# Kernel tuning notes

Measured on AMD Instinct MI355X. Metric: run time of the kernel, lower is better.

The kernel has to match this reference:

```python
import jax, jax.numpy as jnp
import numpy as np

B, S, D, H, DH = 2, 2048, 768, 12, 64
GAMMA = 0.5
SMOOTHING = 1.0  # softmax_attn_smoothing scalar (non-trainable weight in the original)
SCALE = 1.0 / float(np.sqrt(DH))


def setup_inputs() -> dict:
    key = jax.random.key(0)
    ks = jax.random.split(key, 8)
    w = 0.02
    return {
        "inp": jax.random.normal(ks[0], (B, S, D), dtype=jnp.float32),
        "pos_emb": jax.random.normal(ks[1], (S, D), dtype=jnp.float32),
        "Wq_inp": jax.random.normal(ks[2], (D, H * DH), dtype=jnp.float32) * w,
        "Wk_inp": jax.random.normal(ks[3], (D, H * DH), dtype=jnp.float32) * w,
        "Wq_pos": jax.random.normal(ks[4], (D, H * DH), dtype=jnp.float32) * w,
        "Wk_pos": jax.random.normal(ks[5], (D, H * DH), dtype=jnp.float32) * w,
        "Wv": jax.random.normal(ks[6], (D, H * DH), dtype=jnp.float32) * w,
        "Wo": jax.random.normal(ks[7], (H * DH, D), dtype=jnp.float32) * w,
    }


def reference(inp, pos_emb, Wq_inp, Wk_inp, Wq_pos, Wk_pos, Wv, Wo):
    # projections; note original reshape order: [..., d_head, n_head]
    q_i = (inp @ Wq_inp).reshape(B, S, DH, H)
    k_i = (inp @ Wk_inp).reshape(B, S, DH, H)
    q_p = (pos_emb @ Wq_pos).reshape(S, DH, H)
    k_p = (pos_emb @ Wk_pos).reshape(S, DH, H)
    v = (inp @ Wv).reshape(B, S, DH, H)

    # content-content stream: [B,S,S,H], softmax over key axis (axis=2)
    score_inp = jnp.einsum("bidh,bjdh->bijh", q_i, k_i) * (SCALE * SMOOTHING)
    prob_inp = jax.nn.softmax(score_inp, axis=2)

    # position-position stream: [S,S,H], softmax over key axis (axis=1)
    score_pos = jnp.einsum("idh,jdh->ijh", q_p, k_p) * (SCALE * SMOOTHING)
    prob_pos = jax.nn.softmax(score_pos, axis=1)[None]  # [1,S,S,H]

    # gamma blend of the two attention distributions
    attn_prob = (1.0 - GAMMA) * prob_inp + GAMMA * prob_pos  # [B,S,S,H]

    # V-weighted sum, merge heads as [..., h, d] per the original 'bihd' output
    attn_out = jnp.einsum("bijh,bjdh->bihd", attn_prob, v).reshape(B, S, H * DH)
    attn_out = attn_out @ Wo  # [B,S,D]
    return attn_out, attn_prob
```

## Files before the change

### kernel.cpp

```cpp
#include <hip/hip_runtime.h>
#include <hip/hip_bf16.h>

constexpr int NH  = 12;
constexpr int SEQ = 2048;
constexpr int DHD = 64;
constexpr int DIM = 768;
constexpr float QSCALE = 0.125f * 1.44269504088896f;

typedef __bf16 bf16x8 __attribute__((ext_vector_type(8)));
typedef __bf16 bf16x4 __attribute__((ext_vector_type(4)));
typedef float  f32x4  __attribute__((ext_vector_type(4)));

#define MFMA16(a, b, c) __builtin_amdgcn_mfma_f32_16x16x32_bf16((a), (b), (c), 0, 0, 0)

#define LGKM_BARRIER() asm volatile("s_waitcnt lgkmcnt(0)\n\ts_barrier" ::: "memory")

__global__ __launch_bounds__(256) void conv_kernel(
    const float* __restrict__ inp, const float* __restrict__ pos,
    __bf16* __restrict__ Ab, __bf16* __restrict__ Pb)
{
    const int idx = blockIdx.x * 256 + threadIdx.x;
    constexpr int N8I = 4096 * 768 / 8;
    constexpr int N8P = 2048 * 768 / 8;
    if (idx >= N8I + N8P) return;
    const float* src; __bf16* dst; int off;
    if (idx < N8I) { src = inp; dst = Ab; off = idx; }
    else           { src = pos; dst = Pb; off = idx - N8I; }
    const float4 v0 = *reinterpret_cast<const float4*>(&src[(size_t)off * 8]);
    const float4 v1 = *reinterpret_cast<const float4*>(&src[(size_t)off * 8 + 4]);
    bf16x8 t;
    t[0] = (__bf16)v0.x; t[1] = (__bf16)v0.y; t[2] = (__bf16)v0.z; t[3] = (__bf16)v0.w;
    t[4] = (__bf16)v1.x; t[5] = (__bf16)v1.y; t[6] = (__bf16)v1.z; t[7] = (__bf16)v1.w;
    *reinterpret_cast<bf16x8*>(&dst[(size_t)off * 8]) = t;
}

__global__ __launch_bounds__(256) void packw_kernel(
    const float* __restrict__ Wqi, const float* __restrict__ Wki,
    const float* __restrict__ Wvv, const float* __restrict__ Wqp,
    const float* __restrict__ Wkp, __bf16* __restrict__ Wp)
{
    const int kt = blockIdx.x, h = blockIdx.y, z = blockIdx.z;
    const int k0 = kt * 64;
    const float* W; float scale = 1.0f;
    if (z == 0)      { W = Wqi; scale = QSCALE; }
    else if (z == 1) { W = Wki; }
    else if (z == 2) { W = Wvv; }
    else if (z == 3) { W = Wqp; scale = QSCALE; }
    else             { W = Wkp; }

    __shared__ __bf16 lds[64][68];
    const int tid = threadIdx.x;
    {
        const int d = tid & 63, kq = tid >> 6;
        #pragma unroll
        for (int rep = 0; rep < 16; ++rep) {
            const int kk = rep * 4 + kq;
            lds[kk][d] = (__bf16)(W[(size_t)(k0 + kk) * DIM + d * 12 + h] * scale);
        }
    }
    __syncthreads();
    {
        const int k = tid & 63, dq = tid >> 6;
        const size_t slab = ((size_t)z * 12 + h) * 64;
        #pragma unroll
        for (int rep = 0; rep < 16; ++rep) {
            const int d = rep * 4 + dq;
            Wp[(slab + d) * DIM + k0 + k] = lds[k][d];
        }
    }
}

__global__ __launch_bounds__(256) void proj_kernel(
    const __bf16* __restrict__ Ab, const __bf16* __restrict__ Pb,
    const __bf16* __restrict__ Wp,
    __bf16* __restrict__ Qi, __bf16* __restrict__ Ki, __bf16* __restrict__ Vsd,
    __bf16* __restrict__ Qp, __bf16* __restrict__ Kp)
{
    const int bx = blockIdx.x, h = blockIdx.y, z = blockIdx.z;
    if (z >= 3 && bx >= 8) return;
    const int tid = threadIdx.x, lane = tid & 63, wv = tid >> 6;
    const int l15 = lane & 15, lg = lane >> 4;
    const int m_w = bx * 256 + wv * 64;

    const __bf16* Asrc = (z < 3) ? Ab : Pb;
    const __bf16* Wsl = Wp + ((size_t)z * 12 + h) * 64 * DIM;

    f32x4 acc[4][4] = {};

    for (int kt = 0; kt < 24; ++kt) {
        const int k0 = kt * 32;
        bf16x8 a[4], b[4];
        #pragma unroll
        for (int mf = 0; mf < 4; ++mf)
            a[mf] = *reinterpret_cast<const bf16x8*>(
                &Asrc[(size_t)(m_w + mf * 16 + l15) * DIM + k0 + lg * 8]);
        #pragma unroll
        for (int nf = 0; nf < 4; ++nf)
            b[nf] = *reinterpret_cast<const bf16x8*>(
                &Wsl[(size_t)(nf * 16 + l15) * DIM + k0 + lg * 8]);
        #pragma unroll
        for (int mf = 0; mf < 4; ++mf)
            #pragma unroll
            for (int nf = 0; nf < 4; ++nf)
                acc[mf][nf] = MFMA16(a[mf], b[nf], acc[mf][nf]);
    }

    __bf16* outp = (z == 0) ? Qi : (z == 1) ? Ki : (z == 2) ? Vsd : (z == 3) ? Qp : Kp;
    #pragma unroll
    for (int mf = 0; mf < 4; ++mf)
        #pragma unroll
        for (int r = 0; r < 4; ++r) {
            const int m = m_w + mf * 16 + lg * 4 + r;
            const int s = m & 2047;
            const int slab = (z < 3) ? ((m >> 11) * 12 + h) : h;
            const size_t base = ((size_t)slab * SEQ + s) * DHD;
            #pragma unroll
            for (int nf = 0; nf < 4; ++nf)
                outp[base + nf * 16 + l15] = (__bf16)acc[mf][nf][r];
        }
}

__global__ __launch_bounds__(256) void vtrans_kernel(
    const __bf16* __restrict__ Vsd, __bf16* __restrict__ Vt)
{
    const int s0 = blockIdx.x * 64, slab = blockIdx.y;
    __shared__ __bf16 lds[64][66];
    const int tid = threadIdx.x;
    {
        const int rr = tid >> 3, cq = tid & 7;
        #pragma unroll
        for (int rep = 0; rep < 2; ++rep) {
            const int r2 = rr + rep * 32;
            *reinterpret_cast<bf16x8*>(&lds[r2][cq * 8]) =
                *reinterpret_cast<const bf16x8*>(
                    &Vsd[((size_t)slab * SEQ + s0 + r2) * DHD + cq * 8]);
        }
    }
    __syncthreads();
    {
        const int dd = tid >> 3, sq = tid & 7;
        #pragma unroll
        for (int rep = 0; rep < 2; ++rep) {
            const int d2 = dd + rep * 32;
            bf16x8 v;
            #pragma unroll
            for (int q = 0; q < 8; ++q) v[q] = lds[sq * 8 + q][d2];
            *reinterpret_cast<bf16x8*>(&Vt[((size_t)slab * DHD + d2) * SEQ + s0 + sq * 8]) = v;
        }
    }
}

__global__ __launch_bounds__(64) void stats_kernel(
    const __bf16* __restrict__ Qi, const __bf16* __restrict__ Ki,
    const __bf16* __restrict__ Qp, const __bf16* __restrict__ Kp,
    float* __restrict__ m_ws, float* __restrict__ l_ws)
{
    const int bid = blockIdx.x + 128 * (blockIdx.y + 12 * blockIdx.z);
    const int wg = (bid & 7) * 576 + (bid >> 3);
    const int bx = wg & 127, h = (wg >> 7) % 12, bb = wg / 1536;

    const int lane = threadIdx.x;
    const int l15 = lane & 15, lg = lane >> 4;
    const int i0 = bx * 16;

    const __bf16* Q = (bb < 2) ? Qi + ((size_t)bb * NH + h) * SEQ * DHD
                               : Qp + (size_t)h * SEQ * DHD;
    const __bf16* K = (bb < 2) ? Ki + ((size_t)bb * NH + h) * SEQ * DHD
                               : Kp + (size_t)h * SEQ * DHD;

    bf16x8 a[2];
    #pragma unroll
    for (int ks = 0; ks < 2; ++ks)
        a[ks] = *reinterpret_cast<const bf16x8*>(
            &Q[(size_t)(i0 + l15) * DHD + ks * 32 + lg * 8]);

    float mr[4], lr[4];
    #pragma unroll
    for (int r = 0; r < 4; ++r) { mr[r] = -1e30f; lr[r] = 0.0f; }

    for (int jt = 0; jt < 32; ++jt) {
        const int j0 = jt * 64;
        bf16x8 bk[2][4];
        #pragma unroll
        for (int ks = 0; ks < 2; ++ks)
            #pragma unroll
            for (int nf = 0; nf < 4; ++nf)
                bk[ks][nf] = *reinterpret_cast<const bf16x8*>(
                    &K[(size_t)(j0 + nf * 16 + l15) * DHD + ks * 32 + lg * 8]);
        f32x4 c[4] = {};
        #pragma unroll
        for (int ks = 0; ks < 2; ++ks)
            #pragma unroll
            for (int nf = 0; nf < 4; ++nf)
                c[nf] = MFMA16(a[ks], bk[ks][nf], c[nf]);

        #pragma unroll
        for (int r = 0; r < 4; ++r) {
            const float x01 = fmaxf(c[0][r], c[1][r]);
            const float x23 = fmaxf(c[2][r], c[3][r]);
            const float mn = fmaxf(mr[r], fmaxf(x01, x23));
            lr[r] = lr[r] * exp2f(mr[r] - mn)
                  + exp2f(c[0][r] - mn) + exp2f(c[1][r] - mn)
                  + exp2f(c[2][r] - mn) + exp2f(c[3][r] - mn);
            mr[r] = mn;
        }
    }

    #pragma unroll
    for (int msk = 1; msk < 16; msk <<= 1)
        #pragma unroll
        for (int r = 0; r < 4; ++r) {
            const float mo = __shfl_xor(mr[r], msk);
            const float lo = __shfl_xor(lr[r], msk);
            const float mn = fmaxf(mr[r], mo);
            lr[r] = lr[r] * exp2f(mr[r] - mn) + lo * exp2f(mo - mn);
            mr[r] = mn;
        }

    if (l15 == 0) {
        const size_t base = ((size_t)bb * NH + h) * SEQ + i0;
        #pragma unroll
        for (int r = 0; r < 4; ++r) {
            m_ws[base + lg * 4 + r] = mr[r];
            l_ws[base + lg * 4 + r] = lr[r];
        }
    }
}

__global__ __launch_bounds__(384) void emit_kernel(
    const __bf16* __restrict__ Qi, const __bf16* __restrict__ Ki,
    const __bf16* __restrict__ Qp, const __bf16* __restrict__ Kp,
    const __bf16* __restrict__ Vt,
    const float* __restrict__ m_ws, const float* __restrict__ l_ws,
    float* __restrict__ out1, float* __restrict__ attn_pre)
{
    const int bid = blockIdx.x + 128 * (blockIdx.y + 4 * blockIdx.z);
    const int wg = (bid & 7) * 128 + (bid >> 3);
    const int it = wg & 127, js = (wg >> 7) & 3, b = wg >> 9;

    const int i0 = it * 16;
    const int tid = threadIdx.x, lane = tid & 63, wv = tid >> 6;
    const int l15 = lane & 15, lg = lane >> 4;

    __shared__ __align__(16) __bf16 ppv[12][16][40];
    __shared__ __align__(16) __bf16 pb2[16][32][12];
    __shared__ float ml[12][16][4];
    const __bf16* p2flat = &pb2[0][0][0];

    if (tid < 192) {
        const int h = tid >> 4, i = tid & 15;
        const size_t bi  = ((size_t)b * NH + h) * SEQ + i0 + i;
        const size_t ppi = ((size_t)2 * NH + h) * SEQ + i0 + i;
        ml[h][i][0] = m_ws[bi];
        ml[h][i][1] = 0.5f / l_ws[bi];
        ml[h][i][2] = m_ws[ppi];
        ml[h][i][3] = 0.5f / l_ws[ppi];
    }
    __syncthreads();

    const __bf16* Kb[2][2];
    bf16x8 aQ[2][2][2];
    #pragma unroll
    for (int hh = 0; hh < 2; ++hh) {
        const int h = wv * 2 + hh;
        Kb[hh][0] = Ki + ((size_t)b * NH + h) * SEQ * DHD;
        Kb[hh][1] = Kp + (size_t)h * SEQ * DHD;
        #pragma unroll
        for (int ks = 0; ks < 2; ++ks) {
            aQ[hh][0][ks] = *reinterpret_cast<const bf16x8*>(
                &Qi[(((size_t)b * NH + h) * SEQ + i0 + l15) * DHD + ks * 32 + lg * 8]);
            aQ[hh][1][ks] = *reinterpret_cast<const bf16x8*>(
                &Qp[((size_t)h * SEQ + i0 + l15) * DHD + ks * 32 + lg * 8]);
        }
    }

    bf16x8 kf[2][2][2][2];
    {
        const int j0 = js * 512;
        #pragma unroll
        for (int hh = 0; hh < 2; ++hh)
            #pragma unroll
            for (int st = 0; st < 2; ++st)
                #pragma unroll
                for (int nf = 0; nf < 2; ++nf)
                    #pragma unroll
                    for (int ks = 0; ks < 2; ++ks)
                        kf[hh][st][nf][ks] = *reinterpret_cast<const bf16x8*>(
                            &Kb[hh][st][(size_t)(j0 + nf * 16 + l15) * DHD + ks * 32 + lg * 8]);
    }

    f32x4 acc[2][4] = {};

    #pragma unroll 1
    for (int jt = 0; jt < 16; ++jt) {
        const int j0 = js * 512 + jt * 32;
        const int jn = (js * 512 + (jt + 1) * 32) & (SEQ - 1);

        f32x4 ci[2][2] = {}, cq[2][2] = {};
        #pragma unroll
        for (int hh = 0; hh < 2; ++hh)
            #pragma unroll
            for (int ks = 0; ks < 2; ++ks)
                #pragma unroll
                for (int nf = 0; nf < 2; ++nf) {
                    ci[hh][nf] = MFMA16(aQ[hh][0][ks], kf[hh][0][nf][ks], ci[hh][nf]);
                    cq[hh][nf] = MFMA16(aQ[hh][1][ks], kf[hh][1][nf][ks], cq[hh][nf]);
                }

        #pragma unroll
        for (int hh = 0; hh < 2; ++hh)
            #pragma unroll
            for (int st = 0; st < 2; ++st)
                #pragma unroll
                for (int nf = 0; nf < 2; ++nf)
                    #pragma unroll
                    for (int ks = 0; ks < 2; ++ks)
                        kf[hh][st][nf][ks] = *reinterpret_cast<const bf16x8*>(
                            &Kb[hh][st][(size_t)(jn + nf * 16 + l15) * DHD + ks * 32 + lg * 8]);

        #pragma unroll
        for (int hh = 0; hh < 2; ++hh) {
            const int h = wv * 2 + hh;
            #pragma unroll
            for (int r = 0; r < 4; ++r) {
                const int i = lg * 4 + r;
                const f32x4 mlv = *reinterpret_cast<const f32x4*>(&ml[h][i][0]);
                #pragma unroll
                for (int nf = 0; nf < 2; ++nf) {
                    const float pi_ = exp2f(ci[hh][nf][r] - mlv[0]) * mlv[1];
                    const float pq_ = exp2f(cq[hh][nf][r] - mlv[2]) * mlv[3];
                    const __bf16 p = (__bf16)(pi_ + pq_);
                    const int jj = nf * 16 + l15;
                    ppv[h][i][jj] = p;
                    pb2[i][jj][h] = p;
                }
            }
        }

        #pragma unroll
        for (int hh = 0; hh < 2; ++hh) {
            const int h = wv * 2 + hh;
            const bf16x8 ap = *reinterpret_cast<const bf16x8*>(&ppv[h][l15][lg * 8]);
            #pragma unroll
            for (int nf = 0; nf < 4; ++nf) {
                const bf16x8 bv = *reinterpret_cast<const bf16x8*>(
                    &Vt[(((size_t)b * NH + h) * DHD + nf * 16 + l15) * SEQ + j0 + lg * 8]);
                acc[hh][nf] = MFMA16(ap, bv, acc[hh][nf]);
            }
        }

        LGKM_BARRIER();

        #pragma unroll
        for (int k = 0; k < 4; ++k) {
            const int o = (wv * 4 + k) * 256 + 4 * lane;
            const int i = o / 384;
            const int rem = o - i * 384;
            const bf16x4 pv4 = *reinterpret_cast<const bf16x4*>(&p2flat[o]);
            f32x4 v;
            #pragma unroll
            for (int q = 0; q < 4; ++q) v[q] = (float)pv4[q];
            const size_t addr = ((size_t)(b * SEQ + i0 + i) * SEQ + j0) * 12 + rem;
            *reinterpret_cast<f32x4*>(&out1[addr]) = v;
        }

        LGKM_BARRIER();
    }

    #pragma unroll
    for (int hh = 0; hh < 2; ++hh) {
        const int h = wv * 2 + hh;
        #pragma unroll
        for (int nf = 0; nf < 4; ++nf)
            #pragma unroll
            for (int r = 0; r < 4; ++r) {
                const int i = lg * 4 + r;
                atomicAdd(&attn_pre[((size_t)(b * SEQ + i0 + i)) * DIM + h * DHD + nf * 16 + l15],
                          acc[hh][nf][r]);
            }
    }
}

__global__ __launch_bounds__(256) void final_kernel(
    const float* __restrict__ A, const float* __restrict__ W, float* __restrict__ out0)
{
    const int m0 = blockIdx.y * 64;
    const int n0 = blockIdx.x * 192;

    __shared__ __bf16 Al[64][32];
    __shared__ __bf16 Wl[192][32];

    const int tid = threadIdx.x;
    const int lane = tid & 63, wv = tid >> 6;
    const int wm = wv >> 1, wn = wv & 1;
    const int l15 = lane & 15, lg = lane >> 4;

    f32x4 c[2][6] = {};

    for (int kt = 0; kt < 24; ++kt) {
        const int k0 = kt * 32;
        __syncthreads();
        {
            const int r = tid >> 3, kq = tid & 7;
            #pragma unroll
            for (int rep = 0; rep < 2; ++rep) {
                const float4 v = *reinterpret_cast<const float4*>(
                    &A[(size_t)(m0 + r + rep * 32) * DIM + k0 + kq * 4]);
                bf16x4 t;
                t[0] = (__bf16)v.x; t[1] = (__bf16)v.y; t[2] = (__bf16)v.z; t[3] = (__bf16)v.w;
                *reinterpret_cast<bf16x4*>(&Al[r + rep * 32][kq * 4]) = t;
            }
        }
        for (int idx = tid; idx < 32 * 48; idx += 256) {
            const int k = idx / 48, nq = idx - k * 48;
            const float4 v = *reinterpret_cast<const float4*>(
                &W[(size_t)(k0 + k) * DIM + n0 + nq * 4]);
            Wl[nq * 4 + 0][k] = (__bf16)v.x;
            Wl[nq * 4 + 1][k] = (__bf16)v.y;
            Wl[nq * 4 + 2][k] = (__bf16)v.z;
            Wl[nq * 4 + 3][k] = (__bf16)v.w;
        }
        __syncthreads();

        bf16x8 a[2], b[6];
        #pragma unroll
        for (int mf = 0; mf < 2; ++mf)
            a[mf] = *reinterpret_cast<const bf16x8*>(&Al[wm * 32 + mf * 16 + l15][lg * 8]);
        #pragma unroll
        for (int nf = 0; nf < 6; ++nf)
            b[nf] = *reinterpret_cast<const bf16x8*>(&Wl[wn * 96 + nf * 16 + l15][lg * 8]);
        #pragma unroll
        for (int mf = 0; mf < 2; ++mf)
            #pragma unroll
            for (int nf = 0; nf < 6; ++nf)
                c[mf][nf] = MFMA16(a[mf], b[nf], c[mf][nf]);
    }

    #pragma unroll
    for (int mf = 0; mf < 2; ++mf)
        #pragma unroll
        for (int nf = 0; nf < 6; ++nf)
            #pragma unroll
            for (int r = 0; r < 4; ++r) {
                const int m = m0 + wm * 32 + mf * 16 + lg * 4 + r;
                const int n = n0 + wn * 96 + nf * 16 + l15;
                out0[(size_t)m * DIM + n] = c[mf][nf][r];
            }
}

extern "C" void kernel_launch(void* const* d_in, const int* in_sizes, int n_in,
                              void* d_out, int out_size, void* d_ws, size_t ws_size,
                              hipStream_t stream)
{
    (void)in_sizes; (void)n_in; (void)out_size; (void)ws_size;

    const float* inp = (const float*)d_in[0];
    const float* pos = (const float*)d_in[1];
    const float* Wqi = (const float*)d_in[2];
    const float* Wki = (const float*)d_in[3];
    const float* Wqp = (const float*)d_in[4];
    const float* Wkp = (const float*)d_in[5];
    const float* Wvv = (const float*)d_in[6];
    const float* Wo  = (const float*)d_in[7];

    char* w = (char*)d_ws;
    __bf16* Ab = (__bf16*)w;  w += (size_t)4096 * 768 * 2;
    __bf16* Pb = (__bf16*)w;  w += (size_t)2048 * 768 * 2;
    __bf16* Wp = (__bf16*)w;  w += (size_t)5 * 768 * 768 * 2;
    __bf16* Qi = (__bf16*)w;  w += (size_t)2 * NH * SEQ * DHD * 2;
    __bf16* Ki = (__bf16*)w;  w += (size_t)2 * NH * SEQ * DHD * 2;
    __bf16* Vsd = (__bf16*)w; w += (size_t)2 * NH * SEQ * DHD * 2;
    __bf16* Qp = (__bf16*)w;  w += (size_t)NH * SEQ * DHD * 2;
    __bf16* Kp = (__bf16*)w;  w += (size_t)NH * SEQ * DHD * 2;
    float* m_ws = (float*)w;  w += (size_t)3 * NH * SEQ * 4;
    float* l_ws = (float*)w;  w += (size_t)3 * NH * SEQ * 4;
    float* attn_pre = (float*)w; w += (size_t)4096 * DIM * 4;
    __bf16* Vt = Ab;

    float* out0 = (float*)d_out;
    float* out1 = out0 + (size_t)2 * SEQ * DIM;

    hipMemsetAsync(attn_pre, 0, (size_t)4096 * DIM * 4, stream);

    hipLaunchKernelGGL(conv_kernel, dim3(2304), dim3(256), 0, stream, inp, pos, Ab, Pb);
    hipLaunchKernelGGL(packw_kernel, dim3(12, 12, 5), dim3(256), 0, stream,
                       Wqi, Wki, Wvv, Wqp, Wkp, Wp);
    hipLaunchKernelGGL(proj_kernel, dim3(16, 12, 5), dim3(256), 0, stream,
                       Ab, Pb, Wp, Qi, Ki, Vsd, Qp, Kp);
    hipLaunchKernelGGL(vtrans_kernel, dim3(32, 24), dim3(256), 0, stream, Vsd, Vt);
    hipLaunchKernelGGL(stats_kernel, dim3(128, 12, 3), dim3(64), 0, stream,
                       Qi, Ki, Qp, Kp, m_ws, l_ws);
    hipLaunchKernelGGL(emit_kernel, dim3(128, 4, 2), dim3(384), 0, stream,
                       Qi, Ki, Qp, Kp, Vt, m_ws, l_ws, out1, attn_pre);
    hipLaunchKernelGGL(final_kernel, dim3(4, 64, 1), dim3(256), 0, stream,
                       attn_pre, Wo, out0);
}
```

Measured before the change: 718.3 us.

## Split probability emission and PV accumulation into separate kernels

```diff
diff --git a/kernel.cpp b/kernel.cpp
--- a/kernel.cpp
+++ b/kernel.cpp
@@ -12,8 +12,6 @@
 typedef float  f32x4  __attribute__((ext_vector_type(4)));
 
 #define MFMA16(a, b, c) __builtin_amdgcn_mfma_f32_16x16x32_bf16((a), (b), (c), 0, 0, 0)
-
-#define LGKM_BARRIER() asm volatile("s_waitcnt lgkmcnt(0)\n\ts_barrier" ::: "memory")
 
 __global__ __launch_bounds__(256) void conv_kernel(
     const float* __restrict__ inp, const float* __restrict__ pos,
@@ -227,25 +225,23 @@
     }
 }
 
-__global__ __launch_bounds__(384) void emit_kernel(
+__global__ __launch_bounds__(256) void emit_kernel(
     const __bf16* __restrict__ Qi, const __bf16* __restrict__ Ki,
     const __bf16* __restrict__ Qp, const __bf16* __restrict__ Kp,
-    const __bf16* __restrict__ Vt,
     const float* __restrict__ m_ws, const float* __restrict__ l_ws,
-    float* __restrict__ out1, float* __restrict__ attn_pre)
-{
-    const int bid = blockIdx.x + 128 * (blockIdx.y + 4 * blockIdx.z);
+    float* __restrict__ out1)
+{
+    const int bid = blockIdx.x;
     const int wg = (bid & 7) * 128 + (bid >> 3);
-    const int it = wg & 127, js = (wg >> 7) & 3, b = wg >> 9;
+    const int it = wg & 127, jsg = (wg >> 7) & 3, b = wg >> 9;
 
     const int i0 = it * 16;
     const int tid = threadIdx.x, lane = tid & 63, wv = tid >> 6;
     const int l15 = lane & 15, lg = lane >> 4;
-
-    __shared__ __align__(16) __bf16 ppv[12][16][40];
-    __shared__ __align__(16) __bf16 pb2[16][32][12];
+    const int js = jsg * 4 + wv;
+
+    __shared__ __align__(16) __bf16 pbuf[4][16][32][12];
     __shared__ float ml[12][16][4];
-    const __bf16* p2flat = &pb2[0][0][0];
 
     if (tid < 192) {
         const int h = tid >> 4, i = tid & 15;
@@ -258,127 +254,150 @@
     }
     __syncthreads();
 
-    const __bf16* Kb[2][2];
-    bf16x8 aQ[2][2][2];
-    #pragma unroll
-    for (int hh = 0; hh < 2; ++hh) {
-        const int h = wv * 2 + hh;
-        Kb[hh][0] = Ki + ((size_t)b * NH + h) * SEQ * DHD;
-        Kb[hh][1] = Kp + (size_t)h * SEQ * DHD;
-        #pragma unroll
-        for (int ks = 0; ks < 2; ++ks) {
-            aQ[hh][0][ks] = *reinterpret_cast<const bf16x8*>(
-                &Qi[(((size_t)b * NH + h) * SEQ + i0 + l15) * DHD + ks * 32 + lg * 8]);
-            aQ[hh][1][ks] = *reinterpret_cast<const bf16x8*>(
-                &Qp[((size_t)h * SEQ + i0 + l15) * DHD + ks * 32 + lg * 8]);
-        }
-    }
-
-    bf16x8 kf[2][2][2][2];
-    {
-        const int j0 = js * 512;
-        #pragma unroll
-        for (int hh = 0; hh < 2; ++hh)
-            #pragma unroll
-            for (int st = 0; st < 2; ++st)
-                #pragma unroll
-                for (int nf = 0; nf < 2; ++nf)
-                    #pragma unroll
-                    for (int ks = 0; ks < 2; ++ks)
-                        kf[hh][st][nf][ks] = *reinterpret_cast<const bf16x8*>(
-                            &Kb[hh][st][(size_t)(j0 + nf * 16 + l15) * DHD + ks * 32 + lg * 8]);
-    }
-
-    f32x4 acc[2][4] = {};
+    const __bf16* pf = &pbuf[wv][0][0][0];
 
     #pragma unroll 1
-    for (int jt = 0; jt < 16; ++jt) {
-        const int j0 = js * 512 + jt * 32;
-        const int jn = (js * 512 + (jt + 1) * 32) & (SEQ - 1);
-
-        f32x4 ci[2][2] = {}, cq[2][2] = {};
-        #pragma unroll
-        for (int hh = 0; hh < 2; ++hh)
-            #pragma unroll
-            for (int ks = 0; ks < 2; ++ks)
+    for (int jt = 0; jt < 4; ++jt) {
+        const int j0 = js * 128 + jt * 32;
+
+        #pragma unroll 1
+        for (int h = 0; h < 12; ++h) {
+            const __bf16* Qib = Qi + (((size_t)b * NH + h) * SEQ + i0) * DHD;
+            const __bf16* Qpb = Qp + ((size_t)h * SEQ + i0) * DHD;
+            const __bf16* Kib = Ki + ((size_t)b * NH + h) * SEQ * DHD;
+            const __bf16* Kpb = Kp + (size_t)h * SEQ * DHD;
+
+            f32x4 ci[2] = {}, cq[2] = {};
+            #pragma unroll
+            for (int ks = 0; ks < 2; ++ks) {
+                const bf16x8 aQi = *reinterpret_cast<const bf16x8*>(
+                    &Qib[(size_t)l15 * DHD + ks * 32 + lg * 8]);
+                const bf16x8 aQp = *reinterpret_cast<const bf16x8*>(
+                    &Qpb[(size_t)l15 * DHD + ks * 32 + lg * 8]);
                 #pragma unroll
                 for (int nf = 0; nf < 2; ++nf) {
-                    ci[hh][nf] = MFMA16(aQ[hh][0][ks], kf[hh][0][nf][ks], ci[hh][nf]);
-                    cq[hh][nf] = MFMA16(aQ[hh][1][ks], kf[hh][1][nf][ks], cq[hh][nf]);
+                    const bf16x8 bi_ = *reinterpret_cast<const bf16x8*>(
+                        &Kib[(size_t)(j0 + nf * 16 + l15) * DHD + ks * 32 + lg * 8]);
+                    const bf16x8 bp_ = *reinterpret_cast<const bf16x8*>(
+                        &Kpb[(size_t)(j0 + nf * 16 + l15) * DHD + ks * 32 + lg * 8]);
+                    ci[nf] = MFMA16(aQi, bi_, ci[nf]);
+                    cq[nf] = MFMA16(aQp, bp_, cq[nf]);
                 }
-
-        #pragma unroll
-        for (int hh = 0; hh < 2; ++hh)
-            #pragma unroll
-            for (int st = 0; st < 2; ++st)
-                #pragma unroll
-                for (int nf = 0; nf < 2; ++nf)
-                    #pragma unroll
-                    for (int ks = 0; ks < 2; ++ks)
-                        kf[hh][st][nf][ks] = *reinterpret_cast<const bf16x8*>(
-                            &Kb[hh][st][(size_t)(jn + nf * 16 + l15) * DHD + ks * 32 + lg * 8]);
-
-        #pragma unroll
-        for (int hh = 0; hh < 2; ++hh) {
-            const int h = wv * 2 + hh;
+            }
+
             #pragma unroll
             for (int r = 0; r < 4; ++r) {
                 const int i = lg * 4 + r;
                 const f32x4 mlv = *reinterpret_cast<const f32x4*>(&ml[h][i][0]);
                 #pragma unroll
                 for (int nf = 0; nf < 2; ++nf) {
-                    const float pi_ = exp2f(ci[hh][nf][r] - mlv[0]) * mlv[1];
-                    const float pq_ = exp2f(cq[hh][nf][r] - mlv[2]) * mlv[3];
-                    const __bf16 p = (__bf16)(pi_ + pq_);
-                    const int jj = nf * 16 + l15;
-                    ppv[h][i][jj] = p;
-                    pb2[i][jj][h] = p;
+                    const float pi_ = exp2f(ci[nf][r] - mlv[0]) * mlv[1];
+                    const float pq_ = exp2f(cq[nf][r] - mlv[2]) * mlv[3];
+                    pbuf[wv][i][nf * 16 + l15][h] = (__bf16)(pi_ + pq_);
                 }
             }
         }
 
         #pragma unroll
-        for (int hh = 0; hh < 2; ++hh) {
-            const int h = wv * 2 + hh;
-            const bf16x8 ap = *reinterpret_cast<const bf16x8*>(&ppv[h][l15][lg * 8]);
-            #pragma unroll
-            for (int nf = 0; nf < 4; ++nf) {
-                const bf16x8 bv = *reinterpret_cast<const bf16x8*>(
-                    &Vt[(((size_t)b * NH + h) * DHD + nf * 16 + l15) * SEQ + j0 + lg * 8]);
-                acc[hh][nf] = MFMA16(ap, bv, acc[hh][nf]);
-            }
-        }
-
-        LGKM_BARRIER();
-
-        #pragma unroll
-        for (int k = 0; k < 4; ++k) {
-            const int o = (wv * 4 + k) * 256 + 4 * lane;
+        for (int k = 0; k < 24; ++k) {
+            const int o = k * 256 + 4 * lane;
             const int i = o / 384;
             const int rem = o - i * 384;
-            const bf16x4 pv4 = *reinterpret_cast<const bf16x4*>(&p2flat[o]);
+            const bf16x4 pv4 = *reinterpret_cast<const bf16x4*>(&pf[o]);
             f32x4 v;
             #pragma unroll
             for (int q = 0; q < 4; ++q) v[q] = (float)pv4[q];
             const size_t addr = ((size_t)(b * SEQ + i0 + i) * SEQ + j0) * 12 + rem;
             *reinterpret_cast<f32x4*>(&out1[addr]) = v;
         }
-
-        LGKM_BARRIER();
-    }
-
-    #pragma unroll
-    for (int hh = 0; hh < 2; ++hh) {
-        const int h = wv * 2 + hh;
-        #pragma unroll
-        for (int nf = 0; nf < 4; ++nf)
-            #pragma unroll
-            for (int r = 0; r < 4; ++r) {
-                const int i = lg * 4 + r;
-                atomicAdd(&attn_pre[((size_t)(b * SEQ + i0 + i)) * DIM + h * DHD + nf * 16 + l15],
-                          acc[hh][nf][r]);
+    }
+}
+
+__global__ __launch_bounds__(256) void pv_kernel(
+    const __bf16* __restrict__ Qi, const __bf16* __restrict__ Ki,
+    const __bf16* __restrict__ Qp, const __bf16* __restrict__ Kp,
+    const __bf16* __restrict__ Vt,
+    const float* __restrict__ m_ws, const float* __restrict__ l_ws,
+    float* __restrict__ attn_pre)
+{
+    const int itb = blockIdx.x, slab = blockIdx.y;
+    const int b = slab / 12, h = slab - b * 12;
+    const int tid = threadIdx.x, lane = tid & 63, wv = tid >> 6;
+    const int l15 = lane & 15, lg = lane >> 4;
+    const int i0 = itb * 64 + wv * 16;
+
+    const __bf16* Qib = Qi + (((size_t)b * NH + h) * SEQ + i0) * DHD;
+    const __bf16* Qpb = Qp + ((size_t)h * SEQ + i0) * DHD;
+    const __bf16* Kib = Ki + ((size_t)b * NH + h) * SEQ * DHD;
+    const __bf16* Kpb = Kp + (size_t)h * SEQ * DHD;
+    const __bf16* Vtb = Vt + ((size_t)b * NH + h) * DHD * SEQ;
+
+    float mi[4], si[4], mp[4], sp[4];
+    #pragma unroll
+    for (int r = 0; r < 4; ++r) {
+        const int i = i0 + lg * 4 + r;
+        mi[r] = m_ws[((size_t)b * NH + h) * SEQ + i];
+        si[r] = 0.5f / l_ws[((size_t)b * NH + h) * SEQ + i];
+        mp[r] = m_ws[((size_t)2 * NH + h) * SEQ + i];
+        sp[r] = 0.5f / l_ws[((size_t)2 * NH + h) * SEQ + i];
+    }
+
+    bf16x8 aQi[2], aQp[2];
+    #pragma unroll
+    for (int ks = 0; ks < 2; ++ks) {
+        aQi[ks] = *reinterpret_cast<const bf16x8*>(
+            &Qib[(size_t)l15 * DHD + ks * 32 + lg * 8]);
+        aQp[ks] = *reinterpret_cast<const bf16x8*>(
+            &Qpb[(size_t)l15 * DHD + ks * 32 + lg * 8]);
+    }
+
+    __shared__ __align__(16) __bf16 ppv[4][16][40];
+    f32x4 acc[4] = {};
+
+    #pragma unroll 1
+    for (int jt = 0; jt < 64; ++jt) {
+        const int j0 = jt * 32;
+
+        f32x4 ci[2] = {}, cq[2] = {};
+        #pragma unroll
+        for (int ks = 0; ks < 2; ++ks)
+            #pragma unroll
+            for (int nf = 0; nf < 2; ++nf) {
+                const bf16x8 bi_ = *reinterpret_cast<const bf16x8*>(
+                    &Kib[(size_t)(j0 + nf * 16 + l15) * DHD + ks * 32 + lg * 8]);
+                const bf16x8 bp_ = *reinterpret_cast<const bf16x8*>(
+                    &Kpb[(size_t)(j0 + nf * 16 + l15) * DHD + ks * 32 + lg * 8]);
+                ci[nf] = MFMA16(aQi[ks], bi_, ci[nf]);
+                cq[nf] = MFMA16(aQp[ks], bp_, cq[nf]);
             }
-    }
+
+        #pragma unroll
+        for (int r = 0; r < 4; ++r) {
+            const int i = lg * 4 + r;
+            #pragma unroll
+            for (int nf = 0; nf < 2; ++nf) {
+                const float pi_ = exp2f(ci[nf][r] - mi[r]) * si[r];
+                const float pq_ = exp2f(cq[nf][r] - mp[r]) * sp[r];
+                ppv[wv][i][nf * 16 + l15] = (__bf16)(pi_ + pq_);
+            }
+        }
+
+        const bf16x8 ap = *reinterpret_cast<const bf16x8*>(&ppv[wv][l15][lg * 8]);
+        #pragma unroll
+        for (int nf = 0; nf < 4; ++nf) {
+            const bf16x8 bv = *reinterpret_cast<const bf16x8*>(
+                &Vtb[(size_t)(nf * 16 + l15) * SEQ + j0 + lg * 8]);
+            acc[nf] = MFMA16(ap, bv, acc[nf]);
+        }
+    }
+
+    #pragma unroll
+    for (int nf = 0; nf < 4; ++nf)
+        #pragma unroll
+        for (int r = 0; r < 4; ++r) {
+            const int i = i0 + lg * 4 + r;
+            attn_pre[((size_t)(b * SEQ + i)) * DIM + h * DHD + nf * 16 + l15] = acc[nf][r];
+        }
 }
 
 __global__ __launch_bounds__(256) void final_kernel(
@@ -480,8 +499,6 @@
     float* out0 = (float*)d_out;
     float* out1 = out0 + (size_t)2 * SEQ * DIM;
 
-    hipMemsetAsync(attn_pre, 0, (size_t)4096 * DIM * 4, stream);
-
     hipLaunchKernelGGL(conv_kernel, dim3(2304), dim3(256), 0, stream, inp, pos, Ab, Pb);
     hipLaunchKernelGGL(packw_kernel, dim3(12, 12, 5), dim3(256), 0, stream,
                        Wqi, Wki, Wvv, Wqp, Wkp, Wp);
@@ -490,8 +507,10 @@
     hipLaunchKernelGGL(vtrans_kernel, dim3(32, 24), dim3(256), 0, stream, Vsd, Vt);
     hipLaunchKernelGGL(stats_kernel, dim3(128, 12, 3), dim3(64), 0, stream,
                        Qi, Ki, Qp, Kp, m_ws, l_ws);
-    hipLaunchKernelGGL(emit_kernel, dim3(128, 4, 2), dim3(384), 0, stream,
-                       Qi, Ki, Qp, Kp, Vt, m_ws, l_ws, out1, attn_pre);
+    hipLaunchKernelGGL(emit_kernel, dim3(1024), dim3(256), 0, stream,
+                       Qi, Ki, Qp, Kp, m_ws, l_ws, out1);
+    hipLaunchKernelGGL(pv_kernel, dim3(32, 24), dim3(256), 0, stream,
+                       Qi, Ki, Qp, Kp, Vt, m_ws, l_ws, attn_pre);
     hipLaunchKernelGGL(final_kernel, dim3(4, 64, 1), dim3(256), 0, stream,
                        attn_pre, Wo, out0);
 }
```

Result: slower. 897.7 us (+25.0%).
